# Kernel tuning notes

Hardware: AMD Instinct MI355X
Metric: run time of the kernel (lower is better)

The kernel has to match this reference:

```python
import jax, jax.numpy as jnp
import numpy as np

B, H, W = 8, 128, 128
DIM, HEADS, WS, FF = 192, 8, 8, 2
EPS = 1e-6
HD = DIM // HEADS
L = WS * WS
SCALE = HD ** -0.5


def _rel_index(ws):
    coord = np.stack(np.meshgrid(np.arange(ws), np.arange(ws), indexing='ij')).reshape(2, -1)
    rel = (coord[:, :, None] - coord[:, None, :]).transpose(1, 2, 0)
    rel[..., 0] += ws - 1
    rel[..., 1] += ws - 1
    rel[..., 0] *= 2 * ws - 1
    return rel.sum(-1)

REL_INDEX = jnp.asarray(_rel_index(WS))  # (L, L) int


def _part(x):
    # (B,C,H,W) -> (B*nH*nW, L, C)
    b, c, h, w = x.shape
    x = x.reshape(b, c, h // WS, WS, w // WS, WS).transpose(0, 2, 4, 3, 5, 1)
    return x.reshape(-1, L, c)


def _merge(xw, c):
    # (B*nH*nW, L, C) -> (B,C,H,W)
    x = xw.reshape(B, H // WS, W // WS, WS, WS, c).transpose(0, 5, 1, 3, 2, 4)
    return x.reshape(B, c, H, W)


def _forward(x_rgb, x_sar, gamma, beta, ln1_w, ln1_b, ln2_w, ln2_b,
             qkv_w, qkv_b, attn_proj_w, attn_proj_b, rel_bias,
             q_w, kv_w, cross_proj_w, cross_proj_b, ffn_w1, ffn_w2):
    def cln(x, w, b_):
        # conditional LayerNorm over channel dim
        mu = x.mean(axis=1, keepdims=True)
        var = ((x - mu) ** 2).mean(axis=1, keepdims=True)
        xn = (x - mu) * jax.lax.rsqrt(var + EPS)
        xn = xn * w[None, :, None, None] + b_[None, :, None, None]
        return gamma[:, :, None, None] * xn + beta[:, :, None, None]

    def mh(t):  # (n,L,C) -> (n,L,H,hd)
        return t.reshape(t.shape[0], L, HEADS, HD)

    # --- window self-attention with relative position bias ---
    xw = _part(cln(x_rgb, ln1_w, ln1_b))
    qkv = xw @ qkv_w.T + qkv_b
    q, k, v = jnp.split(qkv, 3, axis=-1)
    att = jnp.einsum('nqhd,nkhd->nhqk', mh(q), mh(k)) * SCALE
    bias = rel_bias[REL_INDEX].transpose(2, 0, 1)[None]  # (1,H,L,L)
    att = jax.nn.softmax(att + bias, axis=-1)
    o = jnp.einsum('nhqk,nkhd->nqhd', att, mh(v)).reshape(-1, L, DIM)
    y = jnp.einsum('bchw,oc->bohw', _merge(o, DIM), attn_proj_w) + attn_proj_b[None, :, None, None]
    x1 = x_rgb + y

    # --- windowed cross-attention (q from rgb branch, kv from sar) ---
    qw = _part(cln(x1, ln1_w, ln1_b)) @ q_w.T
    kc, vc = jnp.split(_part(x_sar) @ kv_w.T, 2, axis=-1)
    att2 = jax.nn.softmax(jnp.einsum('nqhd,nkhd->nhqk', mh(qw), mh(kc)) * SCALE, axis=-1)
    o2 = jnp.einsum('nhqk,nkhd->nqhd', att2, mh(vc)).reshape(-1, L, DIM)
    y2 = jnp.einsum('bchw,oc->bohw', _merge(o2, DIM), cross_proj_w) + cross_proj_b[None, :, None, None]
    x2 = x1 + y2

    # --- conv(1x1)-GELU-conv(1x1) FFN ---
    hdn = jax.nn.gelu(jnp.einsum('bchw,oc->bohw', cln(x2, ln2_w, ln2_b), ffn_w1), approximate=False)
    y3 = jnp.einsum('bchw,oc->bohw', hdn, ffn_w2)
    return x2 + y3


def setup_inputs() -> dict:
    key = jax.random.key(0)
    ks = jax.random.split(key, 12)
    d = DIM

    def n(k, shape, s=0.02):
        return jax.random.normal(k, shape, dtype=jnp.float32) * s

    return {
        'x_rgb': jax.random.normal(ks[0], (B, d, H, W), dtype=jnp.float32),
        'x_sar': jax.random.normal(ks[1], (B, d, H, W), dtype=jnp.float32),
        'gamma': jax.random.normal(ks[2], (B, d), dtype=jnp.float32),
        'beta': jax.random.normal(ks[3], (B, d), dtype=jnp.float32),
        'ln1_w': jnp.ones((d,), jnp.float32), 'ln1_b': jnp.zeros((d,), jnp.float32),
        'ln2_w': jnp.ones((d,), jnp.float32), 'ln2_b': jnp.zeros((d,), jnp.float32),
        'qkv_w': n(ks[4], (3 * d, d)), 'qkv_b': jnp.zeros((3 * d,), jnp.float32),
        'attn_proj_w': n(ks[5], (d, d)), 'attn_proj_b': jnp.zeros((d,), jnp.float32),
        'rel_bias': n(ks[6], ((2 * WS - 1) ** 2, HEADS)),
        'q_w': n(ks[7], (d, d)), 'kv_w': n(ks[8], (2 * d, d)),
        'cross_proj_w': n(ks[9], (d, d)), 'cross_proj_b': jnp.zeros((d,), jnp.float32),
        'ffn_w1': n(ks[10], (d * FF * 2, d)), 'ffn_w2': n(ks[11], (d, d * FF * 2)),
    }


def reference(x_rgb, x_sar, gamma, beta, ln1_w, ln1_b, ln2_w, ln2_b,
              qkv_w, qkv_b, attn_proj_w, attn_proj_b, rel_bias,
              q_w, kv_w, cross_proj_w, cross_proj_b, ffn_w1, ffn_w2):
    return _forward(x_rgb, x_sar, gamma, beta, ln1_w, ln1_b, ln2_w, ln2_b,
                    qkv_w, qkv_b, attn_proj_w, attn_proj_b, rel_bias,
                    q_w, kv_w, cross_proj_w, cross_proj_b, ffn_w1, ffn_w2)
```

## Files before the change

### kernel.cpp

```cpp
#include <hip/hip_runtime.h>
#include <math.h>


#define TPB 256
#define TPB2 512
#define NWIN 2048
#define SCALEF 0.20412414523193154f

typedef __attribute__((ext_vector_type(8))) short bhalf8;
typedef __attribute__((ext_vector_type(4))) float fvec4;

#define MFMA(a, b, c) __builtin_amdgcn_mfma_f32_16x16x32_bf16(a, b, c, 0, 0, 0)

__device__ __forceinline__ short f2bf(float f) {
    unsigned u = __float_as_uint(f);
    u = u + 0x7fffu + ((u >> 16) & 1u);
    return (short)(u >> 16);
}
__device__ __forceinline__ float bf2f(short s) {
    return __uint_as_float(((unsigned)(unsigned short)s) << 16);
}

#define N_QKV 147456
#define N_QC  49152
#define N_KV  98304
#define N_AP  36864
#define N_CP  36864
#define N_W1  147456
#define N_W2  147456
#define W_TOT 663552

#define PW 7424

__global__ __launch_bounds__(TPB) void k0_wprep(
    const float* __restrict__ qkvw, const float* __restrict__ qkvb,
    const float* __restrict__ qw, const float* __restrict__ kvw,
    const float* __restrict__ apw, const float* __restrict__ cpw,
    const float* __restrict__ w1, const float* __restrict__ w2,
    short* __restrict__ Wqkv, short* __restrict__ Wqc, short* __restrict__ Wkv,
    short* __restrict__ Wap, short* __restrict__ Wcp, short* __restrict__ W1b,
    short* __restrict__ W2b, float* __restrict__ qbp)
{
    const int tid = blockIdx.x * TPB + threadIdx.x;
    const int stride = gridDim.x * TPB;
    for (int i = tid; i < N_QKV; i += stride) {
        int tile = i >> 9, pos = i & 511;
        int lane = pos >> 3, j = pos & 7, l16 = lane & 15, g = lane >> 4;
        int h = tile / 36, t2 = tile % 36, nt = t2 / 6, kt = t2 % 6;
        int col = nt * 16 + l16, sub = col >> 5, d = col & 31;
        int k = kt * 32 + g * 8 + j;
        float v = (d < 24) ? qkvw[(sub * 192 + h * 24 + d) * 192 + k] : 0.f;
        Wqkv[i] = f2bf(v);
    }
    for (int i = tid; i < N_QC; i += stride) {
        int tile = i >> 9, pos = i & 511;
        int lane = pos >> 3, j = pos & 7, l16 = lane & 15, g = lane >> 4;
        int h = tile / 12, t2 = tile % 12, nt = t2 / 6, kt = t2 % 6;
        int col = nt * 16 + l16;
        int k = kt * 32 + g * 8 + j;
        float v = (col < 24) ? qw[(h * 24 + col) * 192 + k] : 0.f;
        Wqc[i] = f2bf(v);
    }
    for (int i = tid; i < N_KV; i += stride) {
        int tile = i >> 9, pos = i & 511;
        int lane = pos >> 3, j = pos & 7, l16 = lane & 15, g = lane >> 4;
        int h = tile / 24, t2 = tile % 24, nt = t2 / 6, kt = t2 % 6;
        int col = nt * 16 + l16, sub = col >> 5, d = col & 31;
        int k = kt * 32 + g * 8 + j;
        float v = (d < 24) ? kvw[(sub * 192 + h * 24 + d) * 192 + k] : 0.f;
        Wkv[i] = f2bf(v);
    }
    for (int i = tid; i < N_AP; i += stride) {
        int tile = i >> 9, pos = i & 511;
        int lane = pos >> 3, j = pos & 7, l16 = lane & 15, g = lane >> 4;
        int nt = tile / 6, kt = tile % 6;
        int n = nt * 16 + l16, k = kt * 32 + g * 8 + j;
        Wap[i] = f2bf(apw[n * 192 + k]);
    }
    for (int i = tid; i < N_CP; i += stride) {
        int tile = i >> 9, pos = i & 511;
        int lane = pos >> 3, j = pos & 7, l16 = lane & 15, g = lane >> 4;
        int nt = tile / 6, kt = tile % 6;
        int n = nt * 16 + l16, k = kt * 32 + g * 8 + j;
        Wcp[i] = f2bf(cpw[n * 192 + k]);
    }
    for (int i = tid; i < N_W1; i += stride) {
        int tile = i >> 9, pos = i & 511;
        int lane = pos >> 3, j = pos & 7, l16 = lane & 15, g = lane >> 4;
        int nt = tile / 6, kt = tile % 6;
        int n = nt * 16 + l16, k = kt * 32 + g * 8 + j;
        W1b[i] = f2bf(w1[n * 192 + k]);
    }
    for (int i = tid; i < N_W2; i += stride) {
        int tile = i >> 9, pos = i & 511;
        int lane = pos >> 3, j = pos & 7, l16 = lane & 15, g = lane >> 4;
        int nt = tile / 24, ks = tile % 24;
        int n = nt * 16 + l16, k = ks * 32 + g * 8 + j;
        W2b[i] = f2bf(w2[n * 768 + k]);
    }
    for (int i = tid; i < 768; i += stride) {
        int h = i / 96, col = i % 96, sub = col >> 5, d = col & 31;
        qbp[i] = (d < 24) ? qkvb[sub * 192 + h * 24 + d] : 0.f;
    }
}

__global__ __launch_bounds__(TPB) void k1_prep(
    const float* __restrict__ xrgb, const float* __restrict__ xsar,
    const float* __restrict__ gamma, const float* __restrict__ beta,
    const float* __restrict__ ln1w, const float* __restrict__ ln1b,
    short* __restrict__ Ag, short* __restrict__ Xg, short* __restrict__ Sg)
{
    __shared__ float s_x[64 * 193];
    __shared__ float s_mu[64], s_rs[64];
    const int tid = threadIdx.x;
    const int wid = blockIdx.x;
    const int b = wid >> 8, hb = (wid >> 4) & 15, wb = wid & 15;
    const int xbase = ((b * 192) << 14) + ((hb * 8) << 7) + wb * 8;
    const int tok0 = wid * 12288;

    for (int idx = tid; idx < 12288; idx += TPB) {
        int c = idx >> 6, l = idx & 63;
        s_x[l * 193 + c] = xrgb[xbase + (c << 14) + ((l >> 3) << 7) + (l & 7)];
    }
    __syncthreads();
    {
        int t = tid >> 2, q4 = tid & 3;
        float sum = 0.f, sq = 0.f;
        for (int j = 0; j < 48; j++) {
            float v = s_x[t * 193 + q4 * 48 + j];
            sum += v; sq += v * v;
        }
        sum += __shfl_xor(sum, 1); sum += __shfl_xor(sum, 2);
        sq  += __shfl_xor(sq, 1);  sq  += __shfl_xor(sq, 2);
        float mu = sum * (1.f / 192.f);
        float var = sq * (1.f / 192.f) - mu * mu;
        if (q4 == 0) { s_mu[t] = mu; s_rs[t] = rsqrtf(var + 1e-6f); }
    }
    __syncthreads();
    for (int idx = tid; idx < 12288; idx += TPB) {
        int t = idx / 192, c = idx - t * 192;
        float x = s_x[t * 193 + c];
        Xg[tok0 + idx] = f2bf(x);
        float xn = (x - s_mu[t]) * s_rs[t];
        Ag[tok0 + idx] = f2bf((xn * ln1w[c] + ln1b[c]) * gamma[b * 192 + c] + beta[b * 192 + c]);
    }
    __syncthreads();
    for (int idx = tid; idx < 12288; idx += TPB) {
        int c = idx >> 6, l = idx & 63;
        s_x[l * 193 + c] = xsar[xbase + (c << 14) + ((l >> 3) << 7) + (l & 7)];
    }
    __syncthreads();
    for (int idx = tid; idx < 12288; idx += TPB) {
        int t = idx / 192, c = idx - t * 192;
        Sg[tok0 + idx] = f2bf(s_x[t * 193 + c]);
    }
}

__global__ __launch_bounds__(TPB2, 2) void k2_self(
    short* __restrict__ Ag, short* __restrict__ Xg,
    const short* __restrict__ Wqkv, const float* __restrict__ qbp,
    const short* __restrict__ Wap, const float* __restrict__ apb,
    const float* __restrict__ relb,
    const float* __restrict__ ln1w, const float* __restrict__ ln1b,
    const float* __restrict__ gamma, const float* __restrict__ beta)
{
    __shared__ short s_a[12800];
    __shared__ short s_w8[8 * PW];
    __shared__ short s_rb[1800];
    __shared__ float s_part[512];
    __shared__ float s_mv[128];

    const int tid = threadIdx.x;
    const int wid = blockIdx.x;
    const int b = wid >> 8;
    const int w = tid >> 6;
    const int lane = tid & 63;
    const int g = lane >> 4;
    const int l16 = lane & 15;
    const int fo = lane << 3;
    const int tok0 = wid * 12288;
    short* const sq  = &s_w8[w * PW];
    short* const sk  = sq + 2560;
    short* const svt = sq + 5120;
    short* const sp  = sq;
    short* const so  = sq;
    const fvec4 z4 = {0.f, 0.f, 0.f, 0.f};

#pragma unroll
    for (int t = 0; t < 3; t++) {
        int i = tid + t * TPB2;
        int flat = i << 3, row = flat / 192, col = flat - row * 192;
        *(bhalf8*)&s_a[row * 200 + col] = *(const bhalf8*)&Ag[tok0 + flat];
    }
    for (int i = tid; i < 1800; i += TPB2) s_rb[i] = f2bf(relb[i]);
    __syncthreads();

    {
        const int h = w;
        fvec4 acc[4][6];
#pragma unroll
        for (int mt = 0; mt < 4; mt++)
#pragma unroll
            for (int nt = 0; nt < 6; nt++) acc[mt][nt] = z4;
#pragma unroll
        for (int kt = 0; kt < 6; kt++) {
            bhalf8 af[4];
#pragma unroll
            for (int mt = 0; mt < 4; mt++)
                af[mt] = *(const bhalf8*)&s_a[(mt * 16 + l16) * 200 + kt * 32 + g * 8];
#pragma unroll
            for (int nt = 0; nt < 6; nt++) {
                bhalf8 wf = *(const bhalf8*)&Wqkv[((h * 36 + nt * 6 + kt) << 9) + fo];
#pragma unroll
                for (int mt = 0; mt < 4; mt++)
                    acc[mt][nt] = MFMA(af[mt], wf, acc[mt][nt]);
            }
        }
#pragma unroll
        for (int nt = 0; nt < 6; nt++) {
            float bq = qbp[h * 96 + nt * 16 + l16];
            int d = (nt & 1) * 16 + l16;
#pragma unroll
            for (int mt = 0; mt < 4; mt++)
#pragma unroll
                for (int r = 0; r < 4; r++) {
                    int tok = mt * 16 + g * 4 + r;
                    short bv = f2bf(acc[mt][nt][r] + bq);
                    if (nt < 2)      sq[tok * 40 + d] = bv;
                    else if (nt < 4) sk[tok * 40 + d] = bv;
                    else             svt[d * 72 + tok] = bv;
                }
        }
        fvec4 sacc[4][4];
        {
            bhalf8 qf[4], kf[4];
#pragma unroll
            for (int mt = 0; mt < 4; mt++)
                qf[mt] = *(const bhalf8*)&sq[(mt * 16 + l16) * 40 + g * 8];
#pragma unroll
            for (int nt = 0; nt < 4; nt++)
                kf[nt] = *(const bhalf8*)&sk[(nt * 16 + l16) * 40 + g * 8];
#pragma unroll
            for (int mt = 0; mt < 4; mt++)
#pragma unroll
                for (int nt = 0; nt < 4; nt++)
                    sacc[mt][nt] = MFMA(qf[mt], kf[nt], z4);
        }
#pragma unroll
        for (int mt = 0; mt < 4; mt++) {
            float sv[4][4];
#pragma unroll
            for (int nt = 0; nt < 4; nt++) {
                int n = nt * 16 + l16, ki = n >> 3, kj = n & 7;
#pragma unroll
                for (int r = 0; r < 4; r++) {
                    int qq = mt * 16 + g * 4 + r, qi = qq >> 3, qj = qq & 7;
                    int ridx = (qi - ki + 7) * 15 + (qj - kj + 7);
                    sv[nt][r] = sacc[mt][nt][r] * SCALEF + bf2f(s_rb[ridx * 8 + h]);
                }
            }
#pragma unroll
            for (int r = 0; r < 4; r++) {
                float m = fmaxf(fmaxf(sv[0][r], sv[1][r]), fmaxf(sv[2][r], sv[3][r]));
                m = fmaxf(m, __shfl_xor(m, 1)); m = fmaxf(m, __shfl_xor(m, 2));
                m = fmaxf(m, __shfl_xor(m, 4)); m = fmaxf(m, __shfl_xor(m, 8));
                float s = 0.f;
#pragma unroll
                for (int nt = 0; nt < 4; nt++) { sv[nt][r] = __expf(sv[nt][r] - m); s += sv[nt][r]; }
                s += __shfl_xor(s, 1); s += __shfl_xor(s, 2);
                s += __shfl_xor(s, 4); s += __shfl_xor(s, 8);
                float inv = 1.f / s;
#pragma unroll
                for (int nt = 0; nt < 4; nt++)
                    sp[(mt * 16 + g * 4 + r) * 72 + nt * 16 + l16] = f2bf(sv[nt][r] * inv);
            }
        }
        fvec4 oacc[4][2];
#pragma unroll
        for (int mt = 0; mt < 4; mt++) { oacc[mt][0] = z4; oacc[mt][1] = z4; }
#pragma unroll
        for (int ks = 0; ks < 2; ks++) {
            bhalf8 pf[4];
#pragma unroll
            for (int mt = 0; mt < 4; mt++)
                pf[mt] = *(const bhalf8*)&sp[(mt * 16 + l16) * 72 + ks * 32 + g * 8];
#pragma unroll
            for (int nt = 0; nt < 2; nt++) {
                bhalf8 vf = *(const bhalf8*)&svt[(nt * 16 + l16) * 72 + ks * 32 + g * 8];
#pragma unroll
                for (int mt = 0; mt < 4; mt++)
                    oacc[mt][nt] = MFMA(pf[mt], vf, oacc[mt][nt]);
            }
        }
#pragma unroll
        for (int nt = 0; nt < 2; nt++) {
            int d = nt * 16 + l16;
            if (d < 24) {
#pragma unroll
                for (int mt = 0; mt < 4; mt++)
#pragma unroll
                    for (int r = 0; r < 4; r++)
                        so[(mt * 16 + g * 4 + r) * 24 + d] = f2bf(oacc[mt][nt][r]);
            }
        }
    }
    __syncthreads();

    bhalf8 xst[3]; int xr[3], xc[3];
#pragma unroll
    for (int t = 0; t < 3; t++) {
        int i = tid + t * TPB2;
        int flat = i << 3; xr[t] = flat / 192; xc[t] = flat - xr[t] * 192;
        xst[t] = *(const bhalf8*)&Xg[tok0 + flat];
    }

    const int mh = w & 1, ng = w >> 1;
    fvec4 p[2][3];
#pragma unroll
    for (int m = 0; m < 2; m++)
#pragma unroll
        for (int j = 0; j < 3; j++) p[m][j] = z4;
#pragma unroll
    for (int kt = 0; kt < 6; kt++) {
        int c0 = kt * 32 + g * 8;
        int h0 = c0 / 24, d0 = c0 - h0 * 24;
        bhalf8 of[2];
#pragma unroll
        for (int m = 0; m < 2; m++)
            of[m] = *(const bhalf8*)&s_w8[h0 * PW + ((mh * 2 + m) * 16 + l16) * 24 + d0];
#pragma unroll
        for (int j = 0; j < 3; j++) {
            bhalf8 wf = *(const bhalf8*)&Wap[(((ng * 3 + j) * 6 + kt) << 9) + fo];
#pragma unroll
            for (int m = 0; m < 2; m++)
                p[m][j] = MFMA(of[m], wf, p[m][j]);
        }
    }
#pragma unroll
    for (int t = 0; t < 3; t++)
        *(bhalf8*)&s_a[xr[t] * 200 + xc[t]] = xst[t];
    __syncthreads();

    float xv[2][3][4];
#pragma unroll
    for (int j = 0; j < 3; j++) {
        int col = ng * 48 + j * 16 + l16;
        float ap = apb[col];
#pragma unroll
        for (int m = 0; m < 2; m++)
#pragma unroll
            for (int r = 0; r < 4; r++) {
                int row = (mh * 2 + m) * 16 + g * 4 + r;
                xv[m][j][r] = bf2f(s_a[row * 200 + col]) + p[m][j][r] + ap;
            }
    }
#pragma unroll
    for (int m = 0; m < 2; m++)
#pragma unroll
        for (int r = 0; r < 4; r++) {
            float s1 = xv[m][0][r] + xv[m][1][r] + xv[m][2][r];
            float s2 = xv[m][0][r] * xv[m][0][r] + xv[m][1][r] * xv[m][1][r] + xv[m][2][r] * xv[m][2][r];
            s1 += __shfl_xor(s1, 1); s1 += __shfl_xor(s1, 2); s1 += __shfl_xor(s1, 4); s1 += __shfl_xor(s1, 8);
            s2 += __shfl_xor(s2, 1); s2 += __shfl_xor(s2, 2); s2 += __shfl_xor(s2, 4); s2 += __shfl_xor(s2, 8);
            if (l16 == 0) {
                int row = (mh * 2 + m) * 16 + g * 4 + r;
                s_part[(ng * 64 + row) * 2]     = s1;
                s_part[(ng * 64 + row) * 2 + 1] = s2;
            }
        }
    __syncthreads();
    if (tid < 64) {
        float s1 = s_part[tid * 2] + s_part[(64 + tid) * 2] + s_part[(128 + tid) * 2] + s_part[(192 + tid) * 2];
        float s2 = s_part[tid * 2 + 1] + s_part[(64 + tid) * 2 + 1] + s_part[(128 + tid) * 2 + 1] + s_part[(192 + tid) * 2 + 1];
        float mu = s1 * (1.f / 192.f);
        float var = s2 * (1.f / 192.f) - mu * mu;
        s_mv[tid * 2] = mu;
        s_mv[tid * 2 + 1] = rsqrtf(var + 1e-6f);
    }
    __syncthreads();
#pragma unroll
    for (int j = 0; j < 3; j++) {
        int col = ng * 48 + j * 16 + l16;
        float lw = ln1w[col], lb = ln1b[col], ga = gamma[b * 192 + col], be = beta[b * 192 + col];
#pragma unroll
        for (int m = 0; m < 2; m++)
#pragma unroll
            for (int r = 0; r < 4; r++) {
                int row = (mh * 2 + m) * 16 + g * 4 + r;
                float x = xv[m][j][r];
                s_a[row * 200 + col] = f2bf(x);
                float xn = (x - s_mv[row * 2]) * s_mv[row * 2 + 1];
                s_w8[row * 200 + col] = f2bf((xn * lw + lb) * ga + be);
            }
    }
    __syncthreads();
#pragma unroll
    for (int t = 0; t < 3; t++) {
        int i = tid + t * TPB2;
        int flat = i << 3, row = flat / 192, col = flat - row * 192;
        *(bhalf8*)&Xg[tok0 + flat] = *(const bhalf8*)&s_a[row * 200 + col];
        *(bhalf8*)&Ag[tok0 + flat] = *(const bhalf8*)&s_w8[row * 200 + col];
    }
}

__global__ __launch_bounds__(TPB2, 2) void k3_cross(
    short* __restrict__ Ag, short* __restrict__ Xg, const short* __restrict__ Sg,
    const short* __restrict__ Wqc, const short* __restrict__ Wkv,
    const short* __restrict__ Wcp, const float* __restrict__ cpb,
    const float* __restrict__ ln2w, const float* __restrict__ ln2b,
    const float* __restrict__ gamma, const float* __restrict__ beta)
{
    __shared__ short s_s[12800];
    __shared__ short s_w8[8 * PW];
    __shared__ float s_part[512];
    __shared__ float s_mv[128];

    const int tid = threadIdx.x;
    const int wid = blockIdx.x;
    const int b = wid >> 8;
    const int w = tid >> 6;
    const int lane = tid & 63;
    const int g = lane >> 4;
    const int l16 = lane & 15;
    const int fo = lane << 3;
    const int tok0 = wid * 12288;
    short* const sq  = &s_w8[w * PW];
    short* const sk  = sq + 2560;
    short* const svt = sq + 5120;
    short* const sp  = sq;
    short* const so  = sq;
    const fvec4 z4 = {0.f, 0.f, 0.f, 0.f};

#pragma unroll
    for (int t = 0; t < 3; t++) {
        int i = tid + t * TPB2;
        int flat = i << 3, row = flat / 192, col = flat - row * 192;
        *(bhalf8*)&s_s[row * 200 + col] = *(const bhalf8*)&Sg[tok0 + flat];
    }
    __syncthreads();

    {
        const int h = w;
        fvec4 acc[4][6];
#pragma unroll
        for (int mt = 0; mt < 4; mt++)
#pragma unroll
            for (int nt = 0; nt < 6; nt++) acc[mt][nt] = z4;
#pragma unroll
        for (int kt = 0; kt < 6; kt++) {
            bhalf8 ag[4], sf[4];
#pragma unroll
            for (int mt = 0; mt < 4; mt++) {
                ag[mt] = *(const bhalf8*)&Ag[tok0 + (mt * 16 + l16) * 192 + kt * 32 + g * 8];
                sf[mt] = *(const bhalf8*)&s_s[(mt * 16 + l16) * 200 + kt * 32 + g * 8];
            }
#pragma unroll
            for (int nt = 0; nt < 2; nt++) {
                bhalf8 wf = *(const bhalf8*)&Wqc[((h * 12 + nt * 6 + kt) << 9) + fo];
#pragma unroll
                for (int mt = 0; mt < 4; mt++)
                    acc[mt][nt] = MFMA(ag[mt], wf, acc[mt][nt]);
            }
#pragma unroll
            for (int nt = 0; nt < 2; nt++) {
                bhalf8 wf = *(const bhalf8*)&Wkv[((h * 24 + nt * 6 + kt) << 9) + fo];
#pragma unroll
                for (int mt = 0; mt < 4; mt++)
                    acc[mt][2 + nt] = MFMA(sf[mt], wf, acc[mt][2 + nt]);
            }
#pragma unroll
            for (int nt = 0; nt < 2; nt++) {
                bhalf8 wf = *(const bhalf8*)&Wkv[((h * 24 + (nt + 2) * 6 + kt) << 9) + fo];
#pragma unroll
                for (int mt = 0; mt < 4; mt++)
                    acc[mt][4 + nt] = MFMA(sf[mt], wf, acc[mt][4 + nt]);
            }
        }
#pragma unroll
        for (int nt = 0; nt < 6; nt++) {
            int d = (nt & 1) * 16 + l16;
#pragma unroll
            for (int mt = 0; mt < 4; mt++)
#pragma unroll
                for (int r = 0; r < 4; r++) {
                    int tok = mt * 16 + g * 4 + r;
                    short bv = f2bf(acc[mt][nt][r]);
                    if (nt < 2)      sq[tok * 40 + d] = bv;
                    else if (nt < 4) sk[tok * 40 + d] = bv;
                    else             svt[d * 72 + tok] = bv;
                }
        }
        fvec4 sacc[4][4];
        {
            bhalf8 qf[4], kf[4];
#pragma unroll
            for (int mt = 0; mt < 4; mt++)
                qf[mt] = *(const bhalf8*)&sq[(mt * 16 + l16) * 40 + g * 8];
#pragma unroll
            for (int nt = 0; nt < 4; nt++)
                kf[nt] = *(const bhalf8*)&sk[(nt * 16 + l16) * 40 + g * 8];
#pragma unroll
            for (int mt = 0; mt < 4; mt++)
#pragma unroll
                for (int nt = 0; nt < 4; nt++)
                    sacc[mt][nt] = MFMA(qf[mt], kf[nt], z4);
        }
#pragma unroll
        for (int mt = 0; mt < 4; mt++) {
            float sv[4][4];
#pragma unroll
            for (int nt = 0; nt < 4; nt++)
#pragma unroll
                for (int r = 0; r < 4; r++)
                    sv[nt][r] = sacc[mt][nt][r] * SCALEF;
#pragma unroll
            for (int r = 0; r < 4; r++) {
                float m = fmaxf(fmaxf(sv[0][r], sv[1][r]), fmaxf(sv[2][r], sv[3][r]));
                m = fmaxf(m, __shfl_xor(m, 1)); m = fmaxf(m, __shfl_xor(m, 2));
                m = fmaxf(m, __shfl_xor(m, 4)); m = fmaxf(m, __shfl_xor(m, 8));
                float s = 0.f;
#pragma unroll
                for (int nt = 0; nt < 4; nt++) { sv[nt][r] = __expf(sv[nt][r] - m); s += sv[nt][r]; }
                s += __shfl_xor(s, 1); s += __shfl_xor(s, 2);
                s += __shfl_xor(s, 4); s += __shfl_xor(s, 8);
                float inv = 1.f / s;
#pragma unroll
                for (int nt = 0; nt < 4; nt++)
                    sp[(mt * 16 + g * 4 + r) * 72 + nt * 16 + l16] = f2bf(sv[nt][r] * inv);
            }
        }
        fvec4 oacc[4][2];
#pragma unroll
        for (int mt = 0; mt < 4; mt++) { oacc[mt][0] = z4; oacc[mt][1] = z4; }
#pragma unroll
        for (int ks = 0; ks < 2; ks++) {
            bhalf8 pf[4];
#pragma unroll
            for (int mt = 0; mt < 4; mt++)
                pf[mt] = *(const bhalf8*)&sp[(mt * 16 + l16) * 72 + ks * 32 + g * 8];
#pragma unroll
            for (int nt = 0; nt < 2; nt++) {
                bhalf8 vf = *(const bhalf8*)&svt[(nt * 16 + l16) * 72 + ks * 32 + g * 8];
#pragma unroll
                for (int mt = 0; mt < 4; mt++)
                    oacc[mt][nt] = MFMA(pf[mt], vf, oacc[mt][nt]);
            }
        }
#pragma unroll
        for (int nt = 0; nt < 2; nt++) {
            int d = nt * 16 + l16;
            if (d < 24) {
#pragma unroll
                for (int mt = 0; mt < 4; mt++)
#pragma unroll
                    for (int r = 0; r < 4; r++)
                        so[(mt * 16 + g * 4 + r) * 24 + d] = f2bf(oacc[mt][nt][r]);
            }
        }
    }
    __syncthreads();

    bhalf8 xst[3]; int xr[3], xc[3];
#pragma unroll
    for (int t = 0; t < 3; t++) {
        int i = tid + t * TPB2;
        int flat = i << 3; xr[t] = flat / 192; xc[t] = flat - xr[t] * 192;
        xst[t] = *(const bhalf8*)&Xg[tok0 + flat];
    }

    const int mh = w & 1, ng = w >> 1;
    fvec4 p[2][3];
#pragma unroll
    for (int m = 0; m < 2; m++)
#pragma unroll
        for (int j = 0; j < 3; j++) p[m][j] = z4;
#pragma unroll
    for (int kt = 0; kt < 6; kt++) {
        int c0 = kt * 32 + g * 8;
        int h0 = c0 / 24, d0 = c0 - h0 * 24;
        bhalf8 of[2];
#pragma unroll
        for (int m = 0; m < 2; m++)
            of[m] = *(const bhalf8*)&s_w8[h0 * PW + ((mh * 2 + m) * 16 + l16) * 24 + d0];
#pragma unroll
        for (int j = 0; j < 3; j++) {
            bhalf8 wf = *(const bhalf8*)&Wcp[(((ng * 3 + j) * 6 + kt) << 9) + fo];
#pragma unroll
            for (int m = 0; m < 2; m++)
                p[m][j] = MFMA(of[m], wf, p[m][j]);
        }
    }
#pragma unroll
    for (int t = 0; t < 3; t++)
        *(bhalf8*)&s_s[xr[t] * 200 + xc[t]] = xst[t];
    __syncthreads();

    float xv[2][3][4];
#pragma unroll
    for (int j = 0; j < 3; j++) {
        int col = ng * 48 + j * 16 + l16;
        float cp = cpb[col];
#pragma unroll
        for (int m = 0; m < 2; m++)
#pragma unroll
            for (int r = 0; r < 4; r++) {
                int row = (mh * 2 + m) * 16 + g * 4 + r;
                xv[m][j][r] = bf2f(s_s[row * 200 + col]) + p[m][j][r] + cp;
            }
    }
#pragma unroll
    for (int m = 0; m < 2; m++)
#pragma unroll
        for (int r = 0; r < 4; r++) {
            float s1 = xv[m][0][r] + xv[m][1][r] + xv[m][2][r];
            float s2 = xv[m][0][r] * xv[m][0][r] + xv[m][1][r] * xv[m][1][r] + xv[m][2][r] * xv[m][2][r];
            s1 += __shfl_xor(s1, 1); s1 += __shfl_xor(s1, 2); s1 += __shfl_xor(s1, 4); s1 += __shfl_xor(s1, 8);
            s2 += __shfl_xor(s2, 1); s2 += __shfl_xor(s2, 2); s2 += __shfl_xor(s2, 4); s2 += __shfl_xor(s2, 8);
            if (l16 == 0) {
                int row = (mh * 2 + m) * 16 + g * 4 + r;
                s_part[(ng * 64 + row) * 2]     = s1;
                s_part[(ng * 64 + row) * 2 + 1] = s2;
            }
        }
    __syncthreads();
    if (tid < 64) {
        float s1 = s_part[tid * 2] + s_part[(64 + tid) * 2] + s_part[(128 + tid) * 2] + s_part[(192 + tid) * 2];
        float s2 = s_part[tid * 2 + 1] + s_part[(64 + tid) * 2 + 1] + s_part[(128 + tid) * 2 + 1] + s_part[(192 + tid) * 2 + 1];
        float mu = s1 * (1.f / 192.f);
        float var = s2 * (1.f / 192.f) - mu * mu;
        s_mv[tid * 2] = mu;
        s_mv[tid * 2 + 1] = rsqrtf(var + 1e-6f);
    }
    __syncthreads();
#pragma unroll
    for (int j = 0; j < 3; j++) {
        int col = ng * 48 + j * 16 + l16;
        float lw = ln2w[col], lb = ln2b[col], ga = gamma[b * 192 + col], be = beta[b * 192 + col];
#pragma unroll
        for (int m = 0; m < 2; m++)
#pragma unroll
            for (int r = 0; r < 4; r++) {
                int row = (mh * 2 + m) * 16 + g * 4 + r;
                float x = xv[m][j][r];
                s_s[row * 200 + col] = f2bf(x);
                float xn = (x - s_mv[row * 2]) * s_mv[row * 2 + 1];
                s_w8[row * 200 + col] = f2bf((xn * lw + lb) * ga + be);
            }
    }
    __syncthreads();
#pragma unroll
    for (int t = 0; t < 3; t++) {
        int i = tid + t * TPB2;
        int flat = i << 3, row = flat / 192, col = flat - row * 192;
        *(bhalf8*)&Xg[tok0 + flat] = *(const bhalf8*)&s_s[row * 200 + col];
        *(bhalf8*)&Ag[tok0 + flat] = *(const bhalf8*)&s_w8[row * 200 + col];
    }
}

__global__ __launch_bounds__(TPB) void k4_ffn(
    const short* __restrict__ Ag, const short* __restrict__ Xg,
    const short* __restrict__ W1b, const short* __restrict__ W2b,
    float* __restrict__ out)
{
    __shared__ short s_u[12800];
    __shared__ short s_h[12800];

    const int tid = threadIdx.x;
    const int wid = blockIdx.x;
    const int b = wid >> 8, hb = (wid >> 4) & 15, wb = wid & 15;
    const int xbase = ((b * 192) << 14) + ((hb * 8) << 7) + wb * 8;
    const int w = tid >> 6;
    const int lane = tid & 63;
    const int g = lane >> 4;
    const int l16 = lane & 15;
    const int fo = lane << 3;
    const int tok0 = wid * 12288;
    const fvec4 z4 = {0.f, 0.f, 0.f, 0.f};

    for (int i = tid; i < 1536; i += TPB) {
        int flat = i << 3;
        int t = flat / 192, cc = flat - t * 192;
        *(bhalf8*)&s_u[t * 200 + cc] = *(const bhalf8*)&Ag[tok0 + flat];
    }
    __syncthreads();

    fvec4 yacc[4][3];
#pragma unroll
    for (int mt = 0; mt < 4; mt++)
#pragma unroll
        for (int j = 0; j < 3; j++) yacc[mt][j] = z4;

    for (int c = 0; c < 6; c++) {
        fvec4 hacc[4][2];
#pragma unroll
        for (int mt = 0; mt < 4; mt++) { hacc[mt][0] = z4; hacc[mt][1] = z4; }
#pragma unroll
        for (int kt = 0; kt < 6; kt++) {
            bhalf8 af[4];
#pragma unroll
            for (int mt = 0; mt < 4; mt++)
                af[mt] = *(const bhalf8*)&s_u[(mt * 16 + l16) * 200 + kt * 32 + g * 8];
#pragma unroll
            for (int n2 = 0; n2 < 2; n2++) {
                bhalf8 wf = *(const bhalf8*)&W1b[(((c * 8 + w * 2 + n2) * 6 + kt) << 9) + fo];
#pragma unroll
                for (int mt = 0; mt < 4; mt++)
                    hacc[mt][n2] = MFMA(af[mt], wf, hacc[mt][n2]);
            }
        }
#pragma unroll
        for (int n2 = 0; n2 < 2; n2++) {
            int cc = w * 32 + n2 * 16 + l16;
#pragma unroll
            for (int mt = 0; mt < 4; mt++) {
#pragma unroll
                for (int r = 0; r < 4; r++) {
                    float x = hacc[mt][n2][r];
                    float gl = 0.5f * x * (1.f + erff(x * 0.70710678118654752f));
                    s_h[(mt * 16 + g * 4 + r) * 200 + cc] = f2bf(gl);
                }
            }
        }
        __syncthreads();
#pragma unroll
        for (int ks = 0; ks < 4; ks++) {
            bhalf8 hf[4];
#pragma unroll
            for (int mt = 0; mt < 4; mt++)
                hf[mt] = *(const bhalf8*)&s_h[(mt * 16 + l16) * 200 + ks * 32 + g * 8];
#pragma unroll
            for (int j = 0; j < 3; j++) {
                bhalf8 wf = *(const bhalf8*)&W2b[(((w * 3 + j) * 24 + c * 4 + ks) << 9) + fo];
#pragma unroll
                for (int mt = 0; mt < 4; mt++)
                    yacc[mt][j] = MFMA(hf[mt], wf, yacc[mt][j]);
            }
        }
        __syncthreads();
    }

    for (int i = tid; i < 1536; i += TPB) {
        int flat = i << 3;
        int t = flat / 192, cc = flat - t * 192;
        *(bhalf8*)&s_h[t * 200 + cc] = *(const bhalf8*)&Xg[tok0 + flat];
    }
    __syncthreads();
#pragma unroll
    for (int j = 0; j < 3; j++) {
        int col = (w * 3 + j) * 16 + l16;
#pragma unroll
        for (int mt = 0; mt < 4; mt++) {
#pragma unroll
            for (int r = 0; r < 4; r++) {
                int tok = mt * 16 + g * 4 + r;
                float v = bf2f(s_h[tok * 200 + col]) + yacc[mt][j][r];
                s_u[tok * 200 + col] = f2bf(v);
            }
        }
    }
    __syncthreads();
    for (int i = tid; i < 12288; i += TPB) {
        int cc = i >> 6, l = i & 63;
        out[xbase + (cc << 14) + ((l >> 3) << 7) + (l & 7)] = bf2f(s_u[l * 200 + cc]);
    }
}

extern "C" void kernel_launch(void* const* d_in, const int* in_sizes, int n_in,
                              void* d_out, int out_size, void* d_ws, size_t ws_size,
                              hipStream_t stream) {
    const float* xrgb  = (const float*)d_in[0];
    const float* xsar  = (const float*)d_in[1];
    const float* gamma = (const float*)d_in[2];
    const float* beta  = (const float*)d_in[3];
    const float* ln1w  = (const float*)d_in[4];
    const float* ln1b  = (const float*)d_in[5];
    const float* ln2w  = (const float*)d_in[6];
    const float* ln2b  = (const float*)d_in[7];
    const float* qkvw  = (const float*)d_in[8];
    const float* qkvb  = (const float*)d_in[9];
    const float* apw   = (const float*)d_in[10];
    const float* apb   = (const float*)d_in[11];
    const float* relb  = (const float*)d_in[12];
    const float* qw    = (const float*)d_in[13];
    const float* kvw   = (const float*)d_in[14];
    const float* cpw   = (const float*)d_in[15];
    const float* cpb   = (const float*)d_in[16];
    const float* w1    = (const float*)d_in[17];
    const float* w2    = (const float*)d_in[18];

    char* base = (char*)d_ws;
    short* Wqkv = (short*)base;
    short* Wqc  = Wqkv + N_QKV;
    short* Wkv  = Wqc + N_QC;
    short* Wap  = Wkv + N_KV;
    short* Wcp  = Wap + N_AP;
    short* W1b  = Wcp + N_CP;
    short* W2b  = W1b + N_W1;
    float* qbp  = (float*)(base + (size_t)W_TOT * 2);
    short* Ag   = (short*)(base + (size_t)W_TOT * 2 + 3072);
    short* Xg   = Ag + 25165824;
    short* Sg   = Xg + 25165824;

    float* out = (float*)d_out;

    hipLaunchKernelGGL(k0_wprep, dim3(256), dim3(TPB), 0, stream,
                       qkvw, qkvb, qw, kvw, apw, cpw, w1, w2,
                       Wqkv, Wqc, Wkv, Wap, Wcp, W1b, W2b, qbp);
    hipLaunchKernelGGL(k1_prep, dim3(NWIN), dim3(TPB), 0, stream,
                       xrgb, xsar, gamma, beta, ln1w, ln1b, Ag, Xg, Sg);
    hipLaunchKernelGGL(k2_self, dim3(NWIN), dim3(TPB2), 0, stream,
                       Ag, Xg, Wqkv, qbp, Wap, apb, relb, ln1w, ln1b, gamma, beta);
    hipLaunchKernelGGL(k3_cross, dim3(NWIN), dim3(TPB2), 0, stream,
                       Ag, Xg, Sg, Wqc, Wkv, Wcp, cpb, ln2w, ln2b, gamma, beta);
    hipLaunchKernelGGL(k4_ffn, dim3(NWIN), dim3(TPB), 0, stream,
                       Ag, Xg, W1b, W2b, out);
}
```

Before: 971.4 us.

## Vectorize prep/output memory access, add MFMA priority, tanh GELU, prefetch residual

Makes the prep kernel read the NCHW window with float4 loads, stage the LN/conditioning vectors in shared memory, and write the bf16 token tensors as 8-wide vectors. The final FFN kernel prefetches the residual into registers before the main loop and writes its output with float4 stores. MFMA loops in the self- and cross-attention kernels are wrapped with s_setprio. Exact erf GELU is replaced by a tanh-style sigmoid approximation, which changes numerics slightly.

```diff
diff --git a/kernel.cpp b/kernel.cpp
--- a/kernel.cpp
+++ b/kernel.cpp
@@ -112,15 +112,27 @@
 {
     __shared__ float s_x[64 * 193];
     __shared__ float s_mu[64], s_rs[64];
+    __shared__ float s_cw[768];
     const int tid = threadIdx.x;
     const int wid = blockIdx.x;
     const int b = wid >> 8, hb = (wid >> 4) & 15, wb = wid & 15;
     const int xbase = ((b * 192) << 14) + ((hb * 8) << 7) + wb * 8;
     const int tok0 = wid * 12288;
 
-    for (int idx = tid; idx < 12288; idx += TPB) {
-        int c = idx >> 6, l = idx & 63;
-        s_x[l * 193 + c] = xrgb[xbase + (c << 14) + ((l >> 3) << 7) + (l & 7)];
+    for (int i = tid; i < 192; i += TPB) {
+        s_cw[i]       = ln1w[i];
+        s_cw[192 + i] = ln1b[i];
+        s_cw[384 + i] = gamma[b * 192 + i];
+        s_cw[576 + i] = beta[b * 192 + i];
+    }
+    for (int i = tid; i < 3072; i += TPB) {
+        int c = i >> 4, rem = i & 15, hrow = rem >> 1, half = rem & 1;
+        float4 v = *(const float4*)&xrgb[xbase + (c << 14) + (hrow << 7) + half * 4];
+        int l = hrow * 8 + half * 4;
+        s_x[(l + 0) * 193 + c] = v.x;
+        s_x[(l + 1) * 193 + c] = v.y;
+        s_x[(l + 2) * 193 + c] = v.z;
+        s_x[(l + 3) * 193 + c] = v.w;
     }
     __syncthreads();
     {
@@ -137,22 +149,37 @@
         if (q4 == 0) { s_mu[t] = mu; s_rs[t] = rsqrtf(var + 1e-6f); }
     }
     __syncthreads();
-    for (int idx = tid; idx < 12288; idx += TPB) {
-        int t = idx / 192, c = idx - t * 192;
-        float x = s_x[t * 193 + c];
-        Xg[tok0 + idx] = f2bf(x);
-        float xn = (x - s_mu[t]) * s_rs[t];
-        Ag[tok0 + idx] = f2bf((xn * ln1w[c] + ln1b[c]) * gamma[b * 192 + c] + beta[b * 192 + c]);
-    }
-    __syncthreads();
-    for (int idx = tid; idx < 12288; idx += TPB) {
-        int c = idx >> 6, l = idx & 63;
-        s_x[l * 193 + c] = xsar[xbase + (c << 14) + ((l >> 3) << 7) + (l & 7)];
-    }
-    __syncthreads();
-    for (int idx = tid; idx < 12288; idx += TPB) {
-        int t = idx / 192, c = idx - t * 192;
-        Sg[tok0 + idx] = f2bf(s_x[t * 193 + c]);
+    for (int i = tid; i < 1536; i += TPB) {
+        int flat = i << 3, t = flat / 192, c0 = flat - t * 192;
+        float mu = s_mu[t], rs = s_rs[t];
+        bhalf8 xv, av;
+#pragma unroll
+        for (int j = 0; j < 8; j++) {
+            float x = s_x[t * 193 + c0 + j];
+            xv[j] = f2bf(x);
+            float xn = (x - mu) * rs;
+            av[j] = f2bf((xn * s_cw[c0 + j] + s_cw[192 + c0 + j]) * s_cw[384 + c0 + j] + s_cw[576 + c0 + j]);
+        }
+        *(bhalf8*)&Xg[tok0 + flat] = xv;
+        *(bhalf8*)&Ag[tok0 + flat] = av;
+    }
+    __syncthreads();
+    for (int i = tid; i < 3072; i += TPB) {
+        int c = i >> 4, rem = i & 15, hrow = rem >> 1, half = rem & 1;
+        float4 v = *(const float4*)&xsar[xbase + (c << 14) + (hrow << 7) + half * 4];
+        int l = hrow * 8 + half * 4;
+        s_x[(l + 0) * 193 + c] = v.x;
+        s_x[(l + 1) * 193 + c] = v.y;
+        s_x[(l + 2) * 193 + c] = v.z;
+        s_x[(l + 3) * 193 + c] = v.w;
+    }
+    __syncthreads();
+    for (int i = tid; i < 1536; i += TPB) {
+        int flat = i << 3, t = flat / 192, c0 = flat - t * 192;
+        bhalf8 sv;
+#pragma unroll
+        for (int j = 0; j < 8; j++) sv[j] = f2bf(s_x[t * 193 + c0 + j]);
+        *(bhalf8*)&Sg[tok0 + flat] = sv;
     }
 }
 
@@ -202,6 +229,7 @@
         for (int mt = 0; mt < 4; mt++)
 #pragma unroll
             for (int nt = 0; nt < 6; nt++) acc[mt][nt] = z4;
+        __builtin_amdgcn_s_setprio(1);
 #pragma unroll
         for (int kt = 0; kt < 6; kt++) {
             bhalf8 af[4];
@@ -216,6 +244,7 @@
                     acc[mt][nt] = MFMA(af[mt], wf, acc[mt][nt]);
             }
         }
+        __builtin_amdgcn_s_setprio(0);
 #pragma unroll
         for (int nt = 0; nt < 6; nt++) {
             float bq = qbp[h * 96 + nt * 16 + l16];
@@ -446,6 +475,7 @@
         for (int mt = 0; mt < 4; mt++)
 #pragma unroll
             for (int nt = 0; nt < 6; nt++) acc[mt][nt] = z4;
+        __builtin_amdgcn_s_setprio(1);
 #pragma unroll
         for (int kt = 0; kt < 6; kt++) {
             bhalf8 ag[4], sf[4];
@@ -476,6 +506,7 @@
                     acc[mt][4 + nt] = MFMA(sf[mt], wf, acc[mt][4 + nt]);
             }
         }
+        __builtin_amdgcn_s_setprio(0);
 #pragma unroll
         for (int nt = 0; nt < 6; nt++) {
             int d = (nt & 1) * 16 + l16;
@@ -682,6 +713,10 @@
         int t = flat / 192, cc = flat - t * 192;
         *(bhalf8*)&s_u[t * 200 + cc] = *(const bhalf8*)&Ag[tok0 + flat];
     }
+    bhalf8 xpre[6];
+#pragma unroll
+    for (int t6 = 0; t6 < 6; t6++)
+        xpre[t6] = *(const bhalf8*)&Xg[tok0 + ((tid + t6 * TPB) << 3)];
     __syncthreads();
 
     fvec4 yacc[4][3];
@@ -716,7 +751,8 @@
 #pragma unroll
                 for (int r = 0; r < 4; r++) {
                     float x = hacc[mt][n2][r];
-                    float gl = 0.5f * x * (1.f + erff(x * 0.70710678118654752f));
+                    float z = 1.5957691216f * x * (1.f + 0.044715f * x * x);
+                    float gl = x / (1.f + __expf(-z));
                     s_h[(mt * 16 + g * 4 + r) * 200 + cc] = f2bf(gl);
                 }
             }
@@ -739,10 +775,12 @@
         __syncthreads();
     }
 
-    for (int i = tid; i < 1536; i += TPB) {
+#pragma unroll
+    for (int t6 = 0; t6 < 6; t6++) {
+        int i = tid + t6 * TPB;
         int flat = i << 3;
         int t = flat / 192, cc = flat - t * 192;
-        *(bhalf8*)&s_h[t * 200 + cc] = *(const bhalf8*)&Xg[tok0 + flat];
+        *(bhalf8*)&s_h[t * 200 + cc] = xpre[t6];
     }
     __syncthreads();
 #pragma unroll
@@ -759,9 +797,15 @@
         }
     }
     __syncthreads();
-    for (int i = tid; i < 12288; i += TPB) {
-        int cc = i >> 6, l = i & 63;
-        out[xbase + (cc << 14) + ((l >> 3) << 7) + (l & 7)] = bf2f(s_u[l * 200 + cc]);
+    for (int i = tid; i < 3072; i += TPB) {
+        int cc = i >> 4, rem = i & 15, hrow = rem >> 1, half = rem & 1;
+        int l0 = hrow * 8 + half * 4;
+        float4 v;
+        v.x = bf2f(s_u[(l0 + 0) * 200 + cc]);
+        v.y = bf2f(s_u[(l0 + 1) * 200 + cc]);
+        v.z = bf2f(s_u[(l0 + 2) * 200 + cc]);
+        v.w = bf2f(s_u[(l0 + 3) * 200 + cc]);
+        *(float4*)&out[xbase + (cc << 14) + (hrow << 7) + half * 4] = v;
     }
 }
 
```

Measured after the change: 978.6 us. No clear change (+0.7%).
